# Performance work log

Hardware: AMD Instinct MI355X
Metric: run time of the kernel (lower is better)

## Reference

```python
import jax, jax.numpy as jnp
import numpy as np

_FRAC_BITS = 8  # assumed fixed-point fractional bits for bits_quant
_SCALE = float(2 ** _FRAC_BITS)

def bits_quant(x):
    # Simulated fixed-point quantization: round to nearest multiple of 2^-8.
    return jnp.round(x * _SCALE) / _SCALE


def setup_inputs() -> dict:
    key = jax.random.key(0)
    k1, k2, k3 = jax.random.split(key, 3)
    B, D_in, D_out = 4096, 4096, 4096
    inputs = jax.random.normal(k1, (B, D_in), dtype=jnp.float32)
    w = jax.random.normal(k2, (D_in, D_out), dtype=jnp.float32) * 0.02
    b = jax.random.normal(k3, (D_out,), dtype=jnp.float32) * 0.02
    return {"inputs": inputs, "w": w, "b": b}


def reference(inputs, w, b):
    # y = bits_quant(inputs @ w) + bits_quant(b); out = bits_quant(y)
    y = bits_quant(jnp.matmul(inputs, w)) + bits_quant(b)
    return bits_quant(y)
```

## Files before the change

kernel.cpp:

```cpp
#include <hip/hip_runtime.h>
#include <math.h>

typedef __attribute__((ext_vector_type(8))) short   short8;
typedef __attribute__((ext_vector_type(4))) float   f32x4;
typedef __attribute__((ext_vector_type(4))) float   float4v;
typedef __attribute__((ext_vector_type(8))) unsigned short ushort8;
typedef __attribute__((ext_vector_type(4))) unsigned short ushort4v;

#define NDIM 4096

__device__ __forceinline__ unsigned short f2bf(float f) {
  unsigned u = __builtin_bit_cast(unsigned, f);
  u += 0x7fffu + ((u >> 16) & 1u);
  return (unsigned short)(u >> 16);
}

__device__ __forceinline__ void gload_lds16(const unsigned short* g, unsigned short* l) {
  __builtin_amdgcn_global_load_lds(
      (const __attribute__((address_space(1))) void*)g,
      (__attribute__((address_space(3))) void*)l, 16, 0, 0);
}

__global__ void convert_bf16(const float* __restrict__ in, unsigned short* __restrict__ out) {
  int i = (blockIdx.x * blockDim.x + threadIdx.x) * 8;
  float4v a = *(const float4v*)(in + i);
  float4v b = *(const float4v*)(in + i + 4);
  ushort8 o;
  o[0] = f2bf(a[0]); o[1] = f2bf(a[1]); o[2] = f2bf(a[2]); o[3] = f2bf(a[3]);
  o[4] = f2bf(b[0]); o[5] = f2bf(b[1]); o[6] = f2bf(b[2]); o[7] = f2bf(b[3]);
  *(ushort8*)(out + i) = o;
}

__global__ void conv_transpose(const float* __restrict__ W, unsigned short* __restrict__ Wt) {
  __shared__ unsigned short tileb[64][68];
  const int n0 = blockIdx.x * 64, k0 = blockIdx.y * 64;
  const int t  = threadIdx.x;
  const int rr = t >> 4;
  const int cc = (t & 15) * 4;
#pragma unroll
  for (int i = 0; i < 4; ++i) {
    int k = rr + i * 16;
    float4v v = *(const float4v*)&W[(size_t)(k0 + k) * NDIM + n0 + cc];
    ushort4v u;
    u[0] = f2bf(v[0]); u[1] = f2bf(v[1]); u[2] = f2bf(v[2]); u[3] = f2bf(v[3]);
    *(ushort4v*)&tileb[k][cc] = u;
  }
  __syncthreads();
#pragma unroll
  for (int i = 0; i < 2; ++i) {
    int c  = t + i * 256;
    int n  = c >> 3;
    int kc = (c & 7) * 8;
    ushort8 v;
#pragma unroll
    for (int j = 0; j < 8; ++j) v[j] = tileb[kc + j][n];
    *(ushort8*)&Wt[(size_t)(n0 + n) * NDIM + k0 + kc] = v;
  }
}

__global__ void gemm_bt_quant(const unsigned short* __restrict__ A,
                              const unsigned short* __restrict__ Bt,
                              const float* __restrict__ bias,
                              float* __restrict__ C) {
  __shared__ unsigned short As[128 * 32];
  __shared__ unsigned short Bs[128 * 32];

  const int tid  = threadIdx.x;
  const int lane = tid & 63;
  const int wid  = tid >> 6;
  const int wm   = (wid >> 1) * 64;
  const int wn   = (wid & 1) * 64;
  const int m0   = blockIdx.y * 128;
  const int n0   = blockIdx.x * 128;

  const int srow = tid >> 2;
  const int scol = (tid & 3) * 8;
  const unsigned short* Ag0 = A  + (size_t)(m0 + srow)      * NDIM + scol;
  const unsigned short* Ag1 = A  + (size_t)(m0 + 64 + srow) * NDIM + scol;
  const unsigned short* Bg0 = Bt + (size_t)(n0 + srow)      * NDIM + scol;
  const unsigned short* Bg1 = Bt + (size_t)(n0 + 64 + srow) * NDIM + scol;
  unsigned short* As0 = &As[tid * 8];
  unsigned short* As1 = &As[2048 + tid * 8];
  unsigned short* Bs0 = &Bs[tid * 8];
  unsigned short* Bs1 = &Bs[2048 + tid * 8];

  const int frow = lane & 15;
  const int fk   = (lane >> 4) * 8;

  f32x4 acc[4][4] = {};

  for (int kt = 0; kt < NDIM; kt += 32) {
    gload_lds16(Ag0 + kt, As0);
    gload_lds16(Ag1 + kt, As1);
    gload_lds16(Bg0 + kt, Bs0);
    gload_lds16(Bg1 + kt, Bs1);
    __syncthreads();

    short8 af[4], bfr[4];
#pragma unroll
    for (int i = 0; i < 4; ++i)
      af[i] = *(const short8*)&As[(wm + i * 16 + frow) * 32 + fk];
#pragma unroll
    for (int j = 0; j < 4; ++j)
      bfr[j] = *(const short8*)&Bs[(wn + j * 16 + frow) * 32 + fk];
#pragma unroll
    for (int i = 0; i < 4; ++i)
#pragma unroll
      for (int j = 0; j < 4; ++j)
        acc[i][j] = __builtin_amdgcn_mfma_f32_16x16x32_bf16(af[i], bfr[j], acc[i][j], 0, 0, 0);

    __syncthreads();
  }

  const float inv = 1.0f / 256.0f;
  const int colb = n0 + wn + (lane & 15);
  const int rowb = m0 + wm + (lane >> 4) * 4;
#pragma unroll
  for (int j = 0; j < 4; ++j) {
    const int col = colb + j * 16;
    const float qb = rintf(bias[col] * 256.0f) * inv;
#pragma unroll
    for (int i = 0; i < 4; ++i) {
      float* Cp = C + (size_t)(rowb + i * 16) * NDIM + col;
#pragma unroll
      for (int r = 0; r < 4; ++r)
        Cp[(size_t)r * NDIM] = rintf(acc[i][j][r] * 256.0f) * inv + qb;
    }
  }
}

__global__ void gemm_fb(const float* __restrict__ A, const float* __restrict__ W,
                        const float* __restrict__ bias, float* __restrict__ C) {
  __shared__ float As[32][33], Ws[32][33];
  int tx = threadIdx.x, ty = threadIdx.y;
  int m0 = blockIdx.y * 32, n0 = blockIdx.x * 32;
  float acc[4] = {0.f, 0.f, 0.f, 0.f};
  for (int k0 = 0; k0 < NDIM; k0 += 32) {
#pragma unroll
    for (int i = 0; i < 4; ++i) {
      int r = ty + i * 8;
      As[r][tx] = A[(size_t)(m0 + r) * NDIM + k0 + tx];
      Ws[r][tx] = W[(size_t)(k0 + r) * NDIM + n0 + tx];
    }
    __syncthreads();
#pragma unroll
    for (int k = 0; k < 32; ++k) {
      float wv = Ws[k][tx];
#pragma unroll
      for (int i = 0; i < 4; ++i) acc[i] += As[ty + i * 8][k] * wv;
    }
    __syncthreads();
  }
  float qb = rintf(bias[n0 + tx] * 256.0f) * (1.0f / 256.0f);
#pragma unroll
  for (int i = 0; i < 4; ++i)
    C[(size_t)(m0 + ty + i * 8) * NDIM + n0 + tx] =
        rintf(acc[i] * 256.0f) * (1.0f / 256.0f) + qb;
}

extern "C" void kernel_launch(void* const* d_in, const int* in_sizes, int n_in,
                              void* d_out, int out_size, void* d_ws, size_t ws_size,
                              hipStream_t stream) {
  const float* A    = (const float*)d_in[0];
  const float* W    = (const float*)d_in[1];
  const float* bias = (const float*)d_in[2];
  float* C = (float*)d_out;
  const size_t nElem = (size_t)NDIM * NDIM;

  if (ws_size >= nElem * 4) {
    unsigned short* Abf = (unsigned short*)d_ws;
    unsigned short* Wt  = Abf + nElem;
    convert_bf16<<<(int)(nElem / 8 / 256), 256, 0, stream>>>(A, Abf);
    conv_transpose<<<dim3(64, 64), 256, 0, stream>>>(W, Wt);
    gemm_bt_quant<<<dim3(32, 32), 256, 0, stream>>>(Abf, Wt, bias, C);
  } else {
    gemm_fb<<<dim3(128, 128), dim3(32, 8), 0, stream>>>(A, W, bias, C);
  }
}
```

Baseline: 324.3 us.

## Merge prep kernels, double GEMM K-tile with XOR-swizzled LDS, add launch bounds

The A conversion and the W convert-transpose are merged into one prep kernel that selects its role by block index, which saves a kernel launch. The GEMM K-tile grows from 32 to 64, halving the number of barrier pairs per output tile and doing two MFMA sub-steps per LDS fill. An XOR swizzle on the 32-element halves by row parity is meant to cut LDS bank conflicts on fragment reads. A launch-bounds hint of four blocks per CU is added; the doubled LDS footprint (32 KB per block) may reduce occupancy.

```diff
diff --git a/kernel.cpp b/kernel.cpp
--- a/kernel.cpp
+++ b/kernel.cpp
@@ -8,6 +8,7 @@
 typedef __attribute__((ext_vector_type(4))) unsigned short ushort4v;
 
 #define NDIM 4096
+#define BK   64
 
 __device__ __forceinline__ unsigned short f2bf(float f) {
   unsigned u = __builtin_bit_cast(unsigned, f);
@@ -21,49 +22,52 @@
       (__attribute__((address_space(3))) void*)l, 16, 0, 0);
 }
 
-__global__ void convert_bf16(const float* __restrict__ in, unsigned short* __restrict__ out) {
-  int i = (blockIdx.x * blockDim.x + threadIdx.x) * 8;
-  float4v a = *(const float4v*)(in + i);
-  float4v b = *(const float4v*)(in + i + 4);
-  ushort8 o;
-  o[0] = f2bf(a[0]); o[1] = f2bf(a[1]); o[2] = f2bf(a[2]); o[3] = f2bf(a[3]);
-  o[4] = f2bf(b[0]); o[5] = f2bf(b[1]); o[6] = f2bf(b[2]); o[7] = f2bf(b[3]);
-  *(ushort8*)(out + i) = o;
-}
-
-__global__ void conv_transpose(const float* __restrict__ W, unsigned short* __restrict__ Wt) {
+__global__ void prep(const float* __restrict__ A, unsigned short* __restrict__ Abf,
+                     const float* __restrict__ W, unsigned short* __restrict__ Wt) {
   __shared__ unsigned short tileb[64][68];
-  const int n0 = blockIdx.x * 64, k0 = blockIdx.y * 64;
-  const int t  = threadIdx.x;
-  const int rr = t >> 4;
-  const int cc = (t & 15) * 4;
+  const int t = threadIdx.x;
+  if (blockIdx.x < 8192) {
+    int i = (blockIdx.x * 256 + t) * 8;
+    float4v a = *(const float4v*)(A + i);
+    float4v b = *(const float4v*)(A + i + 4);
+    ushort8 o;
+    o[0] = f2bf(a[0]); o[1] = f2bf(a[1]); o[2] = f2bf(a[2]); o[3] = f2bf(a[3]);
+    o[4] = f2bf(b[0]); o[5] = f2bf(b[1]); o[6] = f2bf(b[2]); o[7] = f2bf(b[3]);
+    *(ushort8*)(Abf + i) = o;
+  } else {
+    int b  = blockIdx.x - 8192;
+    int n0 = (b & 63) * 64, k0 = (b >> 6) * 64;
+    const int rr = t >> 4;
+    const int cc = (t & 15) * 4;
 #pragma unroll
-  for (int i = 0; i < 4; ++i) {
-    int k = rr + i * 16;
-    float4v v = *(const float4v*)&W[(size_t)(k0 + k) * NDIM + n0 + cc];
-    ushort4v u;
-    u[0] = f2bf(v[0]); u[1] = f2bf(v[1]); u[2] = f2bf(v[2]); u[3] = f2bf(v[3]);
-    *(ushort4v*)&tileb[k][cc] = u;
-  }
-  __syncthreads();
+    for (int i = 0; i < 4; ++i) {
+      int k = rr + i * 16;
+      float4v v = *(const float4v*)&W[(size_t)(k0 + k) * NDIM + n0 + cc];
+      ushort4v u;
+      u[0] = f2bf(v[0]); u[1] = f2bf(v[1]); u[2] = f2bf(v[2]); u[3] = f2bf(v[3]);
+      *(ushort4v*)&tileb[k][cc] = u;
+    }
+    __syncthreads();
 #pragma unroll
-  for (int i = 0; i < 2; ++i) {
-    int c  = t + i * 256;
-    int n  = c >> 3;
-    int kc = (c & 7) * 8;
-    ushort8 v;
+    for (int i = 0; i < 2; ++i) {
+      int c  = t + i * 256;
+      int n  = c >> 3;
+      int kc = (c & 7) * 8;
+      ushort8 v;
 #pragma unroll
-    for (int j = 0; j < 8; ++j) v[j] = tileb[kc + j][n];
-    *(ushort8*)&Wt[(size_t)(n0 + n) * NDIM + k0 + kc] = v;
+      for (int j = 0; j < 8; ++j) v[j] = tileb[kc + j][n];
+      *(ushort8*)&Wt[(size_t)(n0 + n) * NDIM + k0 + kc] = v;
+    }
   }
 }
 
-__global__ void gemm_bt_quant(const unsigned short* __restrict__ A,
-                              const unsigned short* __restrict__ Bt,
-                              const float* __restrict__ bias,
-                              float* __restrict__ C) {
-  __shared__ unsigned short As[128 * 32];
-  __shared__ unsigned short Bs[128 * 32];
+__global__ __launch_bounds__(256, 4)
+void gemm_bt_quant(const unsigned short* __restrict__ A,
+                   const unsigned short* __restrict__ Bt,
+                   const float* __restrict__ bias,
+                   float* __restrict__ C) {
+  __shared__ unsigned short As[128 * BK];
+  __shared__ unsigned short Bs[128 * BK];
 
   const int tid  = threadIdx.x;
   const int lane = tid & 63;
@@ -73,41 +77,41 @@
   const int m0   = blockIdx.y * 128;
   const int n0   = blockIdx.x * 128;
 
-  const int srow = tid >> 2;
-  const int scol = (tid & 3) * 8;
-  const unsigned short* Ag0 = A  + (size_t)(m0 + srow)      * NDIM + scol;
-  const unsigned short* Ag1 = A  + (size_t)(m0 + 64 + srow) * NDIM + scol;
-  const unsigned short* Bg0 = Bt + (size_t)(n0 + srow)      * NDIM + scol;
-  const unsigned short* Bg1 = Bt + (size_t)(n0 + 64 + srow) * NDIM + scol;
-  unsigned short* As0 = &As[tid * 8];
-  unsigned short* As1 = &As[2048 + tid * 8];
-  unsigned short* Bs0 = &Bs[tid * 8];
-  unsigned short* Bs1 = &Bs[2048 + tid * 8];
+  const int srow = tid >> 3;
+  const int sc   = (tid & 7) ^ ((srow & 1) * 4);
+  const unsigned short* Ag = A  + (size_t)(m0 + srow) * NDIM + sc * 8;
+  const unsigned short* Bg = Bt + (size_t)(n0 + srow) * NDIM + sc * 8;
 
   const int frow = lane & 15;
   const int fk   = (lane >> 4) * 8;
+  const int fpar = frow & 1;
 
   f32x4 acc[4][4] = {};
 
-  for (int kt = 0; kt < NDIM; kt += 32) {
-    gload_lds16(Ag0 + kt, As0);
-    gload_lds16(Ag1 + kt, As1);
-    gload_lds16(Bg0 + kt, Bs0);
-    gload_lds16(Bg1 + kt, Bs1);
+  for (int kt = 0; kt < NDIM; kt += BK) {
+#pragma unroll
+    for (int p = 0; p < 4; ++p) {
+      gload_lds16(Ag + kt + (size_t)p * 32 * NDIM, &As[(p * 256 + tid) * 8]);
+      gload_lds16(Bg + kt + (size_t)p * 32 * NDIM, &Bs[(p * 256 + tid) * 8]);
+    }
     __syncthreads();
 
-    short8 af[4], bfr[4];
 #pragma unroll
-    for (int i = 0; i < 4; ++i)
-      af[i] = *(const short8*)&As[(wm + i * 16 + frow) * 32 + fk];
+    for (int h = 0; h < 2; ++h) {
+      const int ko = fk + 32 * (h ^ fpar);
+      short8 af[4], bfr[4];
 #pragma unroll
-    for (int j = 0; j < 4; ++j)
-      bfr[j] = *(const short8*)&Bs[(wn + j * 16 + frow) * 32 + fk];
-#pragma unroll
-    for (int i = 0; i < 4; ++i)
+      for (int i = 0; i < 4; ++i)
+        af[i] = *(const short8*)&As[(wm + i * 16 + frow) * BK + ko];
 #pragma unroll
       for (int j = 0; j < 4; ++j)
-        acc[i][j] = __builtin_amdgcn_mfma_f32_16x16x32_bf16(af[i], bfr[j], acc[i][j], 0, 0, 0);
+        bfr[j] = *(const short8*)&Bs[(wn + j * 16 + frow) * BK + ko];
+#pragma unroll
+      for (int i = 0; i < 4; ++i)
+#pragma unroll
+        for (int j = 0; j < 4; ++j)
+          acc[i][j] = __builtin_amdgcn_mfma_f32_16x16x32_bf16(af[i], bfr[j], acc[i][j], 0, 0, 0);
+    }
 
     __syncthreads();
   }
@@ -170,8 +174,7 @@
   if (ws_size >= nElem * 4) {
     unsigned short* Abf = (unsigned short*)d_ws;
     unsigned short* Wt  = Abf + nElem;
-    convert_bf16<<<(int)(nElem / 8 / 256), 256, 0, stream>>>(A, Abf);
-    conv_transpose<<<dim3(64, 64), 256, 0, stream>>>(W, Wt);
+    prep<<<8192 + 4096, 256, 0, stream>>>(A, Abf, W, Wt);
     gemm_bt_quant<<<dim3(32, 32), 256, 0, stream>>>(Abf, Wt, bias, C);
   } else {
     gemm_fb<<<dim3(128, 128), dim3(32, 8), 0, stream>>>(A, W, bias, C);
```

After: 311.8 us. 3.8% less time.
